# Kernel tuning notes

Measured on AMD Instinct MI355X. Metric: run time of the kernel, lower is better.

The kernel has to match this reference:

```python
import jax, jax.numpy as jnp
import numpy as np
from jax import lax

B, CEN, CDE, H, W = 4, 256, 256, 64, 64   # de is (B,CDE,H,W); en is (B,CEN,2H,2W)
EMB, K, SCALE = 64, 5, 2
DN = ('NCHW', 'OIHW', 'NCHW')


def conv2d(x, w, b=None, pad=0):
    y = lax.conv_general_dilated(x, w, (1, 1), [(pad, pad), (pad, pad)], dimension_numbers=DN)
    return y if b is None else y + b[None, :, None, None]


def up2(x):
    # F.interpolate(scale_factor=2) default mode='nearest'
    return jnp.repeat(jnp.repeat(x, 2, axis=2), 2, axis=3)


def carafe(de, kernels, k, scale):
    # de: (B,C,H,W); kernels: (B,k*k,H*scale,W*scale), softmax-normalized over dim 1
    b, c, h, w = de.shape
    pad = k // 2
    dep = jnp.pad(de, ((0, 0), (0, 0), (pad, pad), (pad, pad)))
    # (B, C, k*k, H, W): all k*k shifted views of de (zero-padded borders)
    patches = jnp.stack([dep[:, :, dy:dy + h, dx:dx + w]
                         for dy in range(k) for dx in range(k)], axis=2)
    # each output pixel (i,j) reuses the window at source (i//scale, j//scale)
    ker = kernels.reshape(b, k * k, h, scale, w, scale)
    out = jnp.einsum('bkhxwy,bckhw->bchxwy', ker, patches)
    return out.reshape(b, c, h * scale, w * scale)


def xavier_uniform(key, shape):
    fan_out = shape[0] * shape[2] * shape[3]
    fan_in = shape[1] * shape[2] * shape[3]
    limit = float(np.sqrt(6.0 / (fan_in + fan_out)))
    return jax.random.uniform(key, shape, jnp.float32, -limit, limit)


def setup_inputs() -> dict:
    key = jax.random.key(0)
    ks = jax.random.split(key, 7)
    return {
        'en': jax.random.normal(ks[0], (B, CEN, 2 * H, 2 * W), jnp.float32),
        'de': jax.random.normal(ks[1], (B, CDE, H, W), jnp.float32),
        'w_gate': xavier_uniform(ks[2], (1, CDE, 1, 1)),
        'b_gate': jnp.zeros((1,), jnp.float32),
        'w_cen': xavier_uniform(ks[3], (EMB, CEN, 1, 1)),
        'b_cen': jnp.zeros((EMB,), jnp.float32),
        'w_cde': xavier_uniform(ks[4], (EMB, CDE, 1, 1)),
        'w_ce': xavier_uniform(ks[5], (K * K, EMB, 3, 3)),
        'b_ce': jnp.zeros((K * K,), jnp.float32),
    }


def reference(en, de, w_gate, b_gate, w_cen, b_cen, w_cde, w_ce, b_ce):
    # GateGenerator: sigmoid(interpolate(conv1x1(de), x2))
    gate = jax.nn.sigmoid(up2(conv2d(de, w_gate, b_gate)))
    # SemiShift: shared 3x3 content encoder on compressed en and upsampled compressed de
    enc = conv2d(en, w_cen, b_cen)
    dec = conv2d(de, w_cde)          # no bias
    logits = conv2d(enc, w_ce, b_ce, pad=1) + up2(conv2d(dec, w_ce, b_ce, pad=1))
    kernels = jax.nn.softmax(logits, axis=1)
    return gate * en + (1.0 - gate) * carafe(de, kernels, K, SCALE)
```

## Files before the change

kernel.cpp:

```cpp
#include <hip/hip_runtime.h>
#include <math.h>

#define BB 4
#define C 256
#define H 64
#define W 64
#define HW 4096
#define HO 128
#define WO 128
#define HWO 16384
#define EMB 64

typedef __bf16 bf16x8 __attribute__((ext_vector_type(8)));
typedef __bf16 bf16x4 __attribute__((ext_vector_type(4)));
typedef float  f32x4  __attribute__((ext_vector_type(4)));

__device__ __forceinline__ f32x4 mfma16(bf16x8 a, bf16x8 b, f32x4 c) {
    return __builtin_amdgcn_mfma_f32_16x16x32_bf16(a, b, c, 0, 0, 0);
}

__global__ void k_prep2(const float* __restrict__ w_cen,
                        const float* __restrict__ w_cde,
                        const float* __restrict__ w_gate,
                        const float* __restrict__ w_ce,
                        __bf16* __restrict__ wbf_cen,
                        __bf16* __restrict__ wdec5,
                        __bf16* __restrict__ w3) {
    for (int idx = blockIdx.x * blockDim.x + threadIdx.x; idx < 16384;
         idx += gridDim.x * blockDim.x)
        wbf_cen[idx] = (__bf16)w_cen[idx];
    for (int idx = blockIdx.x * blockDim.x + threadIdx.x; idx < 20480;
         idx += gridDim.x * blockDim.x) {
        int c = idx & 255, m = (idx >> 8) & 15;
        float v;
        if (idx < 16384) v = w_cde[idx];
        else             v = (m == 0) ? w_gate[c] : 0.f;
        wdec5[idx] = (__bf16)v;
    }
    for (int idx = blockIdx.x * blockDim.x + threadIdx.x; idx < 18432;
         idx += gridDim.x * blockDim.x) {
        int e = idx & 63;
        int m = (idx >> 6) & 15;
        int mt = (idx >> 10) & 1;
        int tap = idx >> 11;
        int q = mt * 16 + m;
        int dy = tap / 3, dx = tap % 3;
        w3[idx] = (q < 25) ? (__bf16)w_ce[((q * EMB + e) * 3 + dy) * 3 + dx]
                           : (__bf16)0.0f;
    }
}

__global__ __launch_bounds__(256) void k_gemm1(
        const float* __restrict__ en, const float* __restrict__ de,
        const __bf16* __restrict__ wbf_cen, const __bf16* __restrict__ wdec5,
        const float* __restrict__ b_cen, const float* __restrict__ b_gate,
        __bf16* __restrict__ enc_t, __bf16* __restrict__ dec_t,
        float* __restrict__ gate_lr) {
    __shared__ float xs[2][32][68];
    int t = threadIdx.x;
    int w = t >> 6, lane = t & 63;
    int n = lane & 15, q = lane >> 4;
    bool isenc = blockIdx.x < 1024;
    const float* X; const __bf16* Wt; __bf16* Y; int plane, px0, b;
    if (isenc) {
        int blk = blockIdx.x; b = blk >> 8; px0 = (blk & 255) << 6;
        X = en + (size_t)b * C * HWO; plane = HWO; Wt = wbf_cen;
        Y = enc_t + (size_t)b * HWO * EMB;
    } else {
        int blk = blockIdx.x - 1024; b = blk >> 6; px0 = (blk & 63) << 6;
        X = de + (size_t)b * C * HW; plane = HW; Wt = wdec5;
        Y = dec_t + (size_t)b * HW * EMB;
    }
    int scc = t >> 4;
    int sp4 = (t & 15) << 2;
    float4 pre[2];
    #pragma unroll
    for (int i = 0; i < 2; i++)
        pre[i] = *(const float4*)(X + (size_t)(i * 16 + scc) * plane + px0 + sp4);
    #pragma unroll
    for (int i = 0; i < 2; i++)
        *(float4*)(&xs[0][i * 16 + scc][sp4]) = pre[i];
    __syncthreads();

    f32x4 acc[4] = {};
    f32x4 accg = {};
    int px = w * 16 + n;
    for (int kc = 0; kc < 8; kc++) {
        int cur = kc & 1;
        if (kc < 7) {
            int c1 = (kc + 1) * 32;
            #pragma unroll
            for (int i = 0; i < 2; i++)
                pre[i] = *(const float4*)(X + (size_t)(c1 + i * 16 + scc) * plane
                                          + px0 + sp4);
        }
        int c0 = kc * 32;
        bf16x8 af[4];
        #pragma unroll
        for (int mt = 0; mt < 4; mt++)
            af[mt] = *(const bf16x8*)(Wt + (size_t)(mt * 16 + n) * C + c0 + q * 8);
        bf16x8 bv;
        #pragma unroll
        for (int j = 0; j < 8; j++)
            bv[j] = (__bf16)xs[cur][q * 8 + j][px];
        #pragma unroll
        for (int mt = 0; mt < 4; mt++)
            acc[mt] = mfma16(af[mt], bv, acc[mt]);
        if (!isenc) {
            bf16x8 ag = *(const bf16x8*)(Wt + (size_t)(64 + n) * C + c0 + q * 8);
            accg = mfma16(ag, bv, accg);
        }
        if (kc < 7) {
            #pragma unroll
            for (int i = 0; i < 2; i++)
                *(float4*)(&xs[cur ^ 1][i * 16 + scc][sp4]) = pre[i];
        }
        __syncthreads();
    }

    int gpx = px0 + px;
    #pragma unroll
    for (int mt = 0; mt < 4; mt++) {
        int e0 = mt * 16 + q * 4;
        bf16x4 ov;
        #pragma unroll
        for (int r = 0; r < 4; r++) {
            float bias = isenc ? b_cen[e0 + r] : 0.f;
            ov[r] = (__bf16)(acc[mt][r] + bias);
        }
        *(bf16x4*)(Y + (size_t)gpx * EMB + e0) = ov;
    }
    if (!isenc && q == 0)
        gate_lr[b * HW + gpx] = 1.f / (1.f + __expf(-(accg[0] + b_gate[0])));
}

__global__ __launch_bounds__(256) void k_conv3m(
        const __bf16* __restrict__ enc_t, const __bf16* __restrict__ dec_t,
        const __bf16* __restrict__ w3, const float* __restrict__ b_ce,
        float* __restrict__ tmp1, float* __restrict__ tmp2) {
    __shared__ __bf16 sfr[8 * 3 * 66 * 8];
    int t = threadIdx.x;
    int w = t >> 6, lane = t & 63;
    int n = lane & 15, q = lane >> 4;
    bool hi = blockIdx.x < 1024;
    const __bf16* src; float* dst; int b, y, width, plane, x0;
    if (hi) {
        int blk = blockIdx.x; b = blk >> 8; int r = blk & 255;
        y = r >> 1; x0 = (r & 1) * 64;
        width = WO; plane = HWO;
        src = enc_t + (size_t)b * HWO * EMB; dst = tmp1;
    } else {
        int blk = blockIdx.x - 1024; b = blk >> 6; y = blk & 63; x0 = 0;
        width = W; plane = HW;
        src = dec_t + (size_t)b * HW * EMB; dst = tmp2;
    }
    bf16x8 zf;
    #pragma unroll
    for (int j = 0; j < 8; j++) zf[j] = (__bf16)0.0f;
    for (int idx = t; idx < 1584; idx += 256) {
        int f = idx & 7;
        int rem = idx >> 3;
        int xloc = rem % 66, row = rem / 66;
        int yy = y + row - 1, xg = x0 - 1 + xloc;
        bf16x8 v = zf;
        if ((unsigned)yy < (unsigned)width && (unsigned)xg < (unsigned)width)
            v = *(const bf16x8*)(src + ((size_t)yy * width + xg) * EMB + f * 8);
        *(bf16x8*)(sfr + (((f * 3) + row) * 66 + xloc) * 8) = v;
    }
    __syncthreads();

    int x = w * 16 + n;
    f32x4 acc[2] = {};
    #pragma unroll
    for (int row = 0; row < 3; row++) {
        #pragma unroll
        for (int dx = 0; dx < 3; dx++) {
            int tap = row * 3 + dx;
            #pragma unroll
            for (int kc = 0; kc < 2; kc++) {
                bf16x8 bv = *(const bf16x8*)(
                    sfr + ((((kc * 4 + q) * 3) + row) * 66 + x + dx) * 8);
                #pragma unroll
                for (int mt = 0; mt < 2; mt++) {
                    bf16x8 av = *(const bf16x8*)(
                        w3 + ((tap * 2 + mt) * 16 + n) * EMB + kc * 32 + q * 8);
                    acc[mt] = mfma16(av, bv, acc[mt]);
                }
            }
        }
    }
    #pragma unroll
    for (int mt = 0; mt < 2; mt++) {
        #pragma unroll
        for (int r = 0; r < 4; r++) {
            int m = mt * 16 + q * 4 + r;
            if (m < 25)
                dst[((size_t)(b * 25 + m)) * plane + y * width + x0 + x] =
                    acc[mt][r] + b_ce[m];
        }
    }
}

__global__ __launch_bounds__(256) void k_softmax(
        const float* __restrict__ tmp1, const float* __restrict__ tmp2,
        float* __restrict__ kbuf) {
    __shared__ float red[4][64];
    int t = threadIdx.x;
    int tx = t & 63, qg = t >> 6;
    int gp = blockIdx.x * 64 + tx;
    int b = gp >> 14, p = gp & 16383;
    int i = p >> 7, j = p & 127;
    int pl = (i >> 1) * W + (j >> 1);
    int hp = (i & 1) * 2 + (j & 1);
    int q0 = qg * 7;
    int nq = (qg < 3) ? 7 : 4;
    float l[7];
    float mx = -1e30f;
    for (int iq = 0; iq < nq; iq++) {
        int qq = q0 + iq;
        l[iq] = tmp1[((size_t)(b * 25 + qq) << 14) + p]
              + tmp2[((size_t)(b * 25 + qq) << 12) + pl];
        mx = fmaxf(mx, l[iq]);
    }
    red[qg][tx] = mx;
    __syncthreads();
    mx = fmaxf(fmaxf(red[0][tx], red[1][tx]), fmaxf(red[2][tx], red[3][tx]));
    float s = 0.f;
    for (int iq = 0; iq < nq; iq++) { l[iq] = __expf(l[iq] - mx); s += l[iq]; }
    __syncthreads();
    red[qg][tx] = s;
    __syncthreads();
    s = red[0][tx] + red[1][tx] + red[2][tx] + red[3][tx];
    float inv = 1.f / s;
    float* kb = kbuf + ((size_t)(b * HW + pl) * 4 + hp) * 28;
    for (int iq = 0; iq < nq; iq++) kb[q0 + iq] = l[iq] * inv;
    if (qg == 3) { kb[25] = 0.f; kb[26] = 0.f; kb[27] = 0.f; }
}

#define NCH 8
__global__ __launch_bounds__(256) void k_final(
        const float* __restrict__ en, const float* __restrict__ de,
        const float* __restrict__ kbuf, const float* __restrict__ gate_lr,
        float* __restrict__ out) {
    __shared__ float sde[NCH][12][36];
    int t = threadIdx.x;
    int x0 = (blockIdx.x & 1) * 32, y0 = (blockIdx.x >> 1) * 8;
    int c0 = blockIdx.y * NCH;
    int b = blockIdx.z;

    const float* dbase = de + ((size_t)b * C + c0) * HW;
    for (int idx = t; idx < NCH * 432; idx += 256) {
        int c = idx / 432, rem = idx % 432;
        int row = rem / 36, col = rem % 36;
        int yy = y0 - 2 + row, xx = x0 - 2 + col;
        float v = 0.f;
        if ((unsigned)yy < (unsigned)H && (unsigned)xx < (unsigned)W)
            v = dbase[(size_t)c * HW + yy * W + xx];
        sde[c][row][col] = v;
    }

    int tx = t & 31, ty = t >> 5;
    int yl = y0 + ty, xl = x0 + tx;
    float kern[4][25];
    const float* kb = kbuf + (size_t)(b * HW + yl * W + xl) * 112;
    #pragma unroll
    for (int hp = 0; hp < 4; hp++) {
        #pragma unroll
        for (int v = 0; v < 6; v++)
            *(float4*)&kern[hp][v * 4] = *(const float4*)(kb + hp * 28 + v * 4);
        kern[hp][24] = kb[hp * 28 + 24];
    }
    float g = gate_lr[b * HW + yl * W + xl];
    float gm = 1.f - g;
    __syncthreads();

    const float* ebase = en + ((size_t)b * C + c0) * HWO + (2 * yl) * WO + 2 * xl;
    float* obase = out + ((size_t)b * C + c0) * HWO + (2 * yl) * WO + 2 * xl;
    #pragma unroll 2
    for (int c = 0; c < NCH; c++) {
        float a0 = 0.f, a1 = 0.f, a2 = 0.f, a3 = 0.f;
        #pragma unroll
        for (int dy = 0; dy < 5; dy++) {
            #pragma unroll
            for (int dx = 0; dx < 5; dx++) {
                float v = sde[c][ty + dy][tx + dx];
                int k = dy * 5 + dx;
                a0 += kern[0][k] * v;
                a1 += kern[1][k] * v;
                a2 += kern[2][k] * v;
                a3 += kern[3][k] * v;
            }
        }
        size_t cc = (size_t)c * HWO;
        float2 e0 = *(const float2*)(ebase + cc);
        float2 e1 = *(const float2*)(ebase + cc + WO);
        float2 o0, o1;
        o0.x = g * e0.x + gm * a0;  o0.y = g * e0.y + gm * a1;
        o1.x = g * e1.x + gm * a2;  o1.y = g * e1.y + gm * a3;
        *(float2*)(obase + cc) = o0;
        *(float2*)(obase + cc + WO) = o1;
    }
}

extern "C" void kernel_launch(void* const* d_in, const int* in_sizes, int n_in,
                              void* d_out, int out_size, void* d_ws, size_t ws_size,
                              hipStream_t stream) {
    const float* en     = (const float*)d_in[0];
    const float* de     = (const float*)d_in[1];
    const float* w_gate = (const float*)d_in[2];
    const float* b_gate = (const float*)d_in[3];
    const float* w_cen  = (const float*)d_in[4];
    const float* b_cen  = (const float*)d_in[5];
    const float* w_cde  = (const float*)d_in[6];
    const float* w_ce   = (const float*)d_in[7];
    const float* b_ce   = (const float*)d_in[8];
    float* out = (float*)d_out;

    __bf16* wsb     = (__bf16*)d_ws;
    __bf16* wbf_cen = wsb;
    __bf16* wdec5   = wbf_cen + 16384;
    __bf16* w3      = wdec5 + 20480;
    __bf16* enc_t   = w3 + 18432;
    __bf16* dec_t   = enc_t + 4194304;
    float* wsf     = (float*)((char*)d_ws + (size_t)(16384 + 20480 + 18432
                              + 4194304 + 1048576) * 2);
    float* tmp1    = wsf;
    float* tmp2    = tmp1 + 1638400;
    float* gate_lr = tmp2 + 409600;
    float* kbuf    = gate_lr + 16384;

    k_prep2<<<80, 256, 0, stream>>>(w_cen, w_cde, w_gate, w_ce,
                                    wbf_cen, wdec5, w3);
    k_gemm1<<<1280, 256, 0, stream>>>(en, de, wbf_cen, wdec5, b_cen, b_gate,
                                      enc_t, dec_t, gate_lr);
    k_conv3m<<<1280, 256, 0, stream>>>(enc_t, dec_t, w3, b_ce, tmp1, tmp2);
    k_softmax<<<1024, 256, 0, stream>>>(tmp1, tmp2, kbuf);
    k_final<<<dim3(16, 32, 4), 256, 0, stream>>>(en, de, kbuf, gate_lr, out);
}
```

Baseline: 250.6 us.

## Rework gemm1 loads, pixel-major logits layout, retile final CARAFE, alias kbuf

```diff
diff --git a/kernel.cpp b/kernel.cpp
--- a/kernel.cpp
+++ b/kernel.cpp
@@ -56,7 +56,6 @@
         const float* __restrict__ b_cen, const float* __restrict__ b_gate,
         __bf16* __restrict__ enc_t, __bf16* __restrict__ dec_t,
         float* __restrict__ gate_lr) {
-    __shared__ float xs[2][32][68];
     int t = threadIdx.x;
     int w = t >> 6, lane = t & 63;
     int n = lane & 15, q = lane >> 4;
@@ -71,54 +70,32 @@
         X = de + (size_t)b * C * HW; plane = HW; Wt = wdec5;
         Y = dec_t + (size_t)b * HW * EMB;
     }
-    int scc = t >> 4;
-    int sp4 = (t & 15) << 2;
-    float4 pre[2];
-    #pragma unroll
-    for (int i = 0; i < 2; i++)
-        pre[i] = *(const float4*)(X + (size_t)(i * 16 + scc) * plane + px0 + sp4);
-    #pragma unroll
-    for (int i = 0; i < 2; i++)
-        *(float4*)(&xs[0][i * 16 + scc][sp4]) = pre[i];
-    __syncthreads();
+    int px = px0 + w * 16 + n;
+    const float* Xp = X + px;
 
     f32x4 acc[4] = {};
     f32x4 accg = {};
-    int px = w * 16 + n;
+    #pragma unroll
     for (int kc = 0; kc < 8; kc++) {
-        int cur = kc & 1;
-        if (kc < 7) {
-            int c1 = (kc + 1) * 32;
-            #pragma unroll
-            for (int i = 0; i < 2; i++)
-                pre[i] = *(const float4*)(X + (size_t)(c1 + i * 16 + scc) * plane
-                                          + px0 + sp4);
-        }
-        int c0 = kc * 32;
-        bf16x8 af[4];
-        #pragma unroll
-        for (int mt = 0; mt < 4; mt++)
-            af[mt] = *(const bf16x8*)(Wt + (size_t)(mt * 16 + n) * C + c0 + q * 8);
+        int c0 = kc * 32 + q * 8;
+        float xv[8];
+        #pragma unroll
+        for (int j = 0; j < 8; j++)
+            xv[j] = Xp[(size_t)(c0 + j) * plane];
         bf16x8 bv;
         #pragma unroll
-        for (int j = 0; j < 8; j++)
-            bv[j] = (__bf16)xs[cur][q * 8 + j][px];
-        #pragma unroll
-        for (int mt = 0; mt < 4; mt++)
-            acc[mt] = mfma16(af[mt], bv, acc[mt]);
+        for (int j = 0; j < 8; j++) bv[j] = (__bf16)xv[j];
+        #pragma unroll
+        for (int mt = 0; mt < 4; mt++) {
+            bf16x8 af = *(const bf16x8*)(Wt + (size_t)(mt * 16 + n) * C + c0);
+            acc[mt] = mfma16(af, bv, acc[mt]);
+        }
         if (!isenc) {
-            bf16x8 ag = *(const bf16x8*)(Wt + (size_t)(64 + n) * C + c0 + q * 8);
+            bf16x8 ag = *(const bf16x8*)(Wt + (size_t)(64 + n) * C + c0);
             accg = mfma16(ag, bv, accg);
         }
-        if (kc < 7) {
-            #pragma unroll
-            for (int i = 0; i < 2; i++)
-                *(float4*)(&xs[cur ^ 1][i * 16 + scc][sp4]) = pre[i];
-        }
-        __syncthreads();
-    }
-
-    int gpx = px0 + px;
+    }
+
     #pragma unroll
     for (int mt = 0; mt < 4; mt++) {
         int e0 = mt * 16 + q * 4;
@@ -128,10 +105,10 @@
             float bias = isenc ? b_cen[e0 + r] : 0.f;
             ov[r] = (__bf16)(acc[mt][r] + bias);
         }
-        *(bf16x4*)(Y + (size_t)gpx * EMB + e0) = ov;
+        *(bf16x4*)(Y + (size_t)px * EMB + e0) = ov;
     }
     if (!isenc && q == 0)
-        gate_lr[b * HW + gpx] = 1.f / (1.f + __expf(-(accg[0] + b_gate[0])));
+        gate_lr[b * HW + px] = 1.f / (1.f + __expf(-(accg[0] + b_gate[0])));
 }
 
 __global__ __launch_bounds__(256) void k_conv3m(
@@ -189,15 +166,24 @@
             }
         }
     }
-    #pragma unroll
-    for (int mt = 0; mt < 2; mt++) {
-        #pragma unroll
-        for (int r = 0; r < 4; r++) {
-            int m = mt * 16 + q * 4 + r;
-            if (m < 25)
-                dst[((size_t)(b * 25 + m)) * plane + y * width + x0 + x] =
-                    acc[mt][r] + b_ce[m];
-        }
+    float* o = dst + ((size_t)b * plane + y * width + x0 + x) * 28;
+    {
+        float4 f;
+        f.x = acc[0][0] + b_ce[q * 4];
+        f.y = acc[0][1] + b_ce[q * 4 + 1];
+        f.z = acc[0][2] + b_ce[q * 4 + 2];
+        f.w = acc[0][3] + b_ce[q * 4 + 3];
+        *(float4*)(o + q * 4) = f;
+    }
+    if (q < 2) {
+        float4 f;
+        f.x = acc[1][0] + b_ce[16 + q * 4];
+        f.y = acc[1][1] + b_ce[16 + q * 4 + 1];
+        f.z = acc[1][2] + b_ce[16 + q * 4 + 2];
+        f.w = acc[1][3] + b_ce[16 + q * 4 + 3];
+        *(float4*)(o + 16 + q * 4) = f;
+    } else if (q == 2) {
+        o[24] = acc[1][0] + b_ce[24];
     }
 }
 
@@ -214,12 +200,12 @@
     int hp = (i & 1) * 2 + (j & 1);
     int q0 = qg * 7;
     int nq = (qg < 3) ? 7 : 4;
+    const float* t1 = tmp1 + (size_t)(b * HWO + p) * 28 + q0;
+    const float* t2 = tmp2 + (size_t)(b * HW + pl) * 28 + q0;
     float l[7];
     float mx = -1e30f;
     for (int iq = 0; iq < nq; iq++) {
-        int qq = q0 + iq;
-        l[iq] = tmp1[((size_t)(b * 25 + qq) << 14) + p]
-              + tmp2[((size_t)(b * 25 + qq) << 12) + pl];
+        l[iq] = t1[iq] + t2[iq];
         mx = fmaxf(mx, l[iq]);
     }
     red[qg][tx] = mx;
@@ -237,20 +223,22 @@
     if (qg == 3) { kb[25] = 0.f; kb[26] = 0.f; kb[27] = 0.f; }
 }
 
-#define NCH 8
+#define NCH 16
 __global__ __launch_bounds__(256) void k_final(
         const float* __restrict__ en, const float* __restrict__ de,
         const float* __restrict__ kbuf, const float* __restrict__ gate_lr,
         float* __restrict__ out) {
-    __shared__ float sde[NCH][12][36];
+    __shared__ float sde[NCH][8][36];
     int t = threadIdx.x;
-    int x0 = (blockIdx.x & 1) * 32, y0 = (blockIdx.x >> 1) * 8;
+    int x0 = (blockIdx.x & 1) * 32, y0 = (blockIdx.x >> 1) * 4;
     int c0 = blockIdx.y * NCH;
     int b = blockIdx.z;
 
     const float* dbase = de + ((size_t)b * C + c0) * HW;
-    for (int idx = t; idx < NCH * 432; idx += 256) {
-        int c = idx / 432, rem = idx % 432;
+    #pragma unroll
+    for (int it = 0; it < 18; it++) {
+        int idx = it * 256 + t;
+        int c = idx / 288, rem = idx % 288;
         int row = rem / 36, col = rem % 36;
         int yy = y0 - 2 + row, xx = x0 - 2 + col;
         float v = 0.f;
@@ -259,46 +247,39 @@
         sde[c][row][col] = v;
     }
 
-    int tx = t & 31, ty = t >> 5;
+    int h = t >> 7;
+    int rem = t & 127;
+    int ty = rem >> 5, tx = rem & 31;
     int yl = y0 + ty, xl = x0 + tx;
-    float kern[4][25];
-    const float* kb = kbuf + (size_t)(b * HW + yl * W + xl) * 112;
-    #pragma unroll
-    for (int hp = 0; hp < 4; hp++) {
-        #pragma unroll
-        for (int v = 0; v < 6; v++)
-            *(float4*)&kern[hp][v * 4] = *(const float4*)(kb + hp * 28 + v * 4);
-        kern[hp][24] = kb[hp * 28 + 24];
-    }
+    float ker[56];
+    const float* kb = kbuf + ((size_t)(b * HW + yl * W + xl) * 4 + 2 * h) * 28;
+    #pragma unroll
+    for (int v = 0; v < 14; v++)
+        *(float4*)&ker[v * 4] = *(const float4*)(kb + v * 4);
     float g = gate_lr[b * HW + yl * W + xl];
     float gm = 1.f - g;
     __syncthreads();
 
-    const float* ebase = en + ((size_t)b * C + c0) * HWO + (2 * yl) * WO + 2 * xl;
-    float* obase = out + ((size_t)b * C + c0) * HWO + (2 * yl) * WO + 2 * xl;
-    #pragma unroll 2
+    const float* ebase = en + ((size_t)b * C + c0) * HWO + (2 * yl + h) * WO + 2 * xl;
+    float* obase = out + ((size_t)b * C + c0) * HWO + (2 * yl + h) * WO + 2 * xl;
     for (int c = 0; c < NCH; c++) {
-        float a0 = 0.f, a1 = 0.f, a2 = 0.f, a3 = 0.f;
+        float a0 = 0.f, a1 = 0.f;
         #pragma unroll
         for (int dy = 0; dy < 5; dy++) {
             #pragma unroll
             for (int dx = 0; dx < 5; dx++) {
                 float v = sde[c][ty + dy][tx + dx];
                 int k = dy * 5 + dx;
-                a0 += kern[0][k] * v;
-                a1 += kern[1][k] * v;
-                a2 += kern[2][k] * v;
-                a3 += kern[3][k] * v;
+                a0 += ker[k] * v;
+                a1 += ker[28 + k] * v;
             }
         }
         size_t cc = (size_t)c * HWO;
         float2 e0 = *(const float2*)(ebase + cc);
-        float2 e1 = *(const float2*)(ebase + cc + WO);
-        float2 o0, o1;
-        o0.x = g * e0.x + gm * a0;  o0.y = g * e0.y + gm * a1;
-        o1.x = g * e1.x + gm * a2;  o1.y = g * e1.y + gm * a3;
+        float2 o0;
+        o0.x = g * e0.x + gm * a0;
+        o0.y = g * e0.y + gm * a1;
         *(float2*)(obase + cc) = o0;
-        *(float2*)(obase + cc + WO) = o1;
     }
 }
 
@@ -325,9 +306,9 @@
     float* wsf     = (float*)((char*)d_ws + (size_t)(16384 + 20480 + 18432
                               + 4194304 + 1048576) * 2);
     float* tmp1    = wsf;
-    float* tmp2    = tmp1 + 1638400;
-    float* gate_lr = tmp2 + 409600;
-    float* kbuf    = gate_lr + 16384;
+    float* tmp2    = tmp1 + 1835008;
+    float* gate_lr = tmp2 + 458752;
+    float* kbuf    = (float*)enc_t;
 
     k_prep2<<<80, 256, 0, stream>>>(w_cen, w_cde, w_gate, w_ce,
                                     wbf_cen, wdec5, w3);
@@ -335,5 +316,5 @@
                                       enc_t, dec_t, gate_lr);
     k_conv3m<<<1280, 256, 0, stream>>>(enc_t, dec_t, w3, b_ce, tmp1, tmp2);
     k_softmax<<<1024, 256, 0, stream>>>(tmp1, tmp2, kbuf);
-    k_final<<<dim3(16, 32, 4), 256, 0, stream>>>(en, de, kbuf, gate_lr, out);
-}
+    k_final<<<dim3(32, 16, 4), 256, 0, stream>>>(en, de, kbuf, gate_lr, out);
+}
```

After: 237.6 us. 5.2% less time.
